# Kernel optimization log

Hardware: AMD Instinct MI355X
Metric: run time of the kernel (lower is better)

## Reference

```python
import jax, jax.numpy as jnp
import numpy as np

FULL_SCALE = 256
THRESH = 15.0  # full_scale > 128 -> distance_threshold = 15


def bilinear_sample(img, x, y):
    # img: [C,Hi,Wi]; x,y: [...] in [-1,1]; align_corners=False, zero padding
    C, Hi, Wi = img.shape
    xg = ((x + 1.0) * Wi - 1.0) / 2.0
    yg = ((y + 1.0) * Hi - 1.0) / 2.0
    x0 = jnp.floor(xg).astype(jnp.int32); x1 = x0 + 1
    y0 = jnp.floor(yg).astype(jnp.int32); y1 = y0 + 1
    wx = xg - x0.astype(img.dtype); wy = yg - y0.astype(img.dtype)

    def gather(yi, xi):
        valid = (yi >= 0) & (yi < Hi) & (xi >= 0) & (xi < Wi)
        yc = jnp.clip(yi, 0, Hi - 1); xc = jnp.clip(xi, 0, Wi - 1)
        return img[:, yc, xc] * valid[None].astype(img.dtype)

    return (gather(y0, x0) * ((1 - wy) * (1 - wx))[None]
            + gather(y0, x1) * ((1 - wy) * wx)[None]
            + gather(y1, x0) * (wy * (1 - wx))[None]
            + gather(y1, x1) * (wy * wx)[None])  # [C, ...]


def setup_inputs() -> dict:
    key = jax.random.key(0)
    k1, k2 = jax.random.split(key)
    image_x = jax.random.normal(k1, (1, 64, 256, 256), dtype=jnp.float32)
    all_edges = jax.random.uniform(k2, (8, 32, 4), dtype=jnp.float32)
    return {"image_x": image_x, "all_edges": all_edges}


def reference(image_x, all_edges):
    H = W = FULL_SCALE
    rows = jnp.arange(H, dtype=image_x.dtype)
    cols = jnp.arange(W, dtype=image_x.dtype)
    Vs, Us = jnp.meshgrid(rows, cols, indexing='ij')
    UV = jnp.stack([Vs, Us], axis=-1)  # [H,W,2] as (row, col), matches torch UVs

    def per_group(edges):
        e = edges * FULL_SCALE
        e0, e1 = e[:, :2], e[:, 2:4]
        d = e1 - e0                                    # [E,2]
        L = jnp.sqrt((d * d).sum(-1))                  # [E]
        dn = d / jnp.maximum(L, 1e-4)[:, None]
        nrm = jnp.stack([dn[:, 1], -dn[:, 0]], -1)     # normals
        diff = UV[:, :, None, :] - e0                  # [H,W,E,2]
        nd = jnp.abs((diff * nrm).sum(-1))             # normal distances [H,W,E]
        dd = (diff * dn).sum(-1) / jnp.maximum(L, 1e-4)  # direction distances
        near0 = jnp.sqrt((diff * diff).sum(-1)) <= THRESH
        near1 = jnp.sqrt(((UV[:, :, None, :] - e1) ** 2).sum(-1)) <= THRESH
        m = ((nd <= THRESH) & (dd <= 1) & (dd >= 0)) | near0 | near1  # all_edge_mask
        edge_mask = m.any(-1)                          # [H,W]
        off = jnp.minimum(dd, 1.0 - dd)                # point offsets
        mf = m.astype(image_x.dtype)
        pinfo = (off * mf).sum(-1) / jnp.maximum(mf.sum(-1), 1e-4)  # [H,W]
        return edge_mask, pinfo

    edge_mask, pinfo = jax.vmap(per_group)(all_edges)  # [G,H,W], [G,H,W]

    # grid_sample at every grid point (dense/masked equivalent of nonzero+gather);
    # torch swaps (v,u)->(u,v) so x = col, y = row, normalized p/size*2-1
    gx = (Us / FULL_SCALE) * 2.0 - 1.0
    gy = (Vs / FULL_SCALE) * 2.0 - 1.0
    sampled = bilinear_sample(image_x[0], gx, gy)      # [C,H,W]
    sampled = jnp.moveaxis(sampled, 0, -1)             # [H,W,C]

    G = all_edges.shape[0]
    feats = jnp.concatenate(
        [jnp.broadcast_to(sampled, (G,) + sampled.shape), pinfo[..., None]], axis=-1)
    feats = feats * edge_mask[..., None].astype(feats.dtype)  # zero non-edge pixels
    return feats, edge_mask
```

## Files before the change

kernel.cpp:

```cpp
#include <hip/hip_runtime.h>

#define HH 256
#define WW 256
#define CC 64
#define NG 8
#define NE 32
#define PX 32
#define THRESH 15.0f

typedef float f32x4 __attribute__((ext_vector_type(4)));

#define FEATS_ELEMS ((size_t)NG * HH * WW * 65)

#define IMG_ELEMS (CC * 2 * 33)

__global__ __launch_bounds__(256, 6) void fused_sparse_encoder(
    const float* __restrict__ img,
    const float* __restrict__ edges,
    float* __restrict__ out)
{
#pragma clang fp contract(off)
    __shared__ float  s_buf[66 * 65];
    __shared__ float4 s_k1[NG * NE];
    __shared__ float2 s_k2[NG * NE];
    __shared__ float  s_k3[NG * NE];
    __shared__ float  s_mask[NG * PX];
    __shared__ float  s_pinfo[NG * PX];

    const int tid = threadIdx.x;
    const int u0  = blockIdx.x * PX;
    const int v   = blockIdx.y;

    {
        const float4 e4 = reinterpret_cast<const float4*>(edges)[tid];
        const float e0v = e4.x * 256.0f;
        const float e0u = e4.y * 256.0f;
        const float e1v = e4.z * 256.0f;
        const float e1u = e4.w * 256.0f;
        const float d0 = e1v - e0v;
        const float d1 = e1u - e0u;
        const float L  = __fsqrt_rn(d0 * d0 + d1 * d1);
        const float Lm = fmaxf(L, 1e-4f);
        s_k1[tid] = make_float4(e0v, e0u, __fdiv_rn(d0, Lm), __fdiv_rn(d1, Lm));
        s_k2[tid] = make_float2(e1v, e1u);
        s_k3[tid] = Lm;
    }
    __syncthreads();

    float cbuf[17];
    #pragma unroll
    for (int t = 0; t < 17; ++t) {
        const int i = tid + t * 256;
        float val = 0.0f;
        if (i < IMG_ELEMS) {
            const int c  = i / 66;
            const int r  = i - c * 66;
            const int yy = r / 33;
            const int x  = r - yy * 33;
            const int gy = v - 1 + yy;
            const int gx = u0 - 1 + x;
            if (gy >= 0 && gx >= 0) {
                val = img[((size_t)c * HH + gy) * WW + gx];
            }
        }
        cbuf[t] = val;
    }

    {
        const int px = tid & (PX - 1);
        const int g  = tid >> 5;
        const float U = (float)(u0 + px);
        const float V = (float)v;
        float sm = 0.0f, cnt = 0.0f;
        bool any = false;
        for (int e = 0; e < NE; ++e) {
            const int idx = g * NE + e;
            const float4 k1 = s_k1[idx];
            const float2 k2 = s_k2[idx];
            const float  Lm = s_k3[idx];
            const float diff0 = V - k1.x;
            const float diff1 = U - k1.y;
            const float ndv = diff0 * k1.w - diff1 * k1.z;
            const float ddn = diff0 * k1.z + diff1 * k1.w;
            const float dd  = __fdiv_rn(ddn, Lm);
            const float r0sq = diff0 * diff0 + diff1 * diff1;
            const float f0 = V - k2.x;
            const float f1 = U - k2.y;
            const float r1sq = f0 * f0 + f1 * f1;
            const bool m = ((fabsf(ndv) <= THRESH) && (dd <= 1.0f) && (dd >= 0.0f))
                           || (r0sq <= 225.0f) || (r1sq <= 225.0f);
            if (m) {
                any = true;
                sm += fminf(dd, 1.0f - dd);
                cnt += 1.0f;
            }
        }
        const float pf = __fdiv_rn(sm, fmaxf(cnt, 1e-4f));
        const float mv = any ? 1.0f : 0.0f;
        s_mask[g * PX + px]  = mv;
        s_pinfo[g * PX + px] = pf;
        out[FEATS_ELEMS + ((size_t)g * HH + v) * WW + (u0 + px)] = mv;
    }

    #pragma unroll
    for (int t = 0; t < 17; ++t) {
        const int i = tid + t * 256;
        if (i < IMG_ELEMS) {
            const int c  = i / 66;
            const int r  = i - c * 66;
            const int yy = r / 33;
            const int x  = r - yy * 33;
            s_buf[(yy * 33 + x) * 65 + c] = cbuf[t];
        }
    }
    __syncthreads();

    const int wv   = tid >> 6;
    const int lane = tid & 63;
    float sreg[8];
    #pragma unroll
    for (int i = 0; i < 8; ++i) {
        const int p = wv * 8 + i;
        sreg[i] = s_buf[(p) * 65 + lane] * 0.25f
                + s_buf[(p + 1) * 65 + lane] * 0.25f
                + s_buf[(33 + p) * 65 + lane] * 0.25f
                + s_buf[(34 + p) * 65 + lane] * 0.25f;
    }
    __syncthreads();

    #pragma unroll
    for (int i = 0; i < 8; ++i) {
        const int p = wv * 8 + i;
        s_buf[p * 65 + lane] = sreg[i];
    }
    __syncthreads();

    for (int g = 0; g < NG; ++g) {
        const float* msk = &s_mask[g * PX];
        const float* pin = &s_pinfo[g * PX];
        float* gout = out + (((size_t)g * HH + v) * WW + u0) * 65;
        #pragma unroll
        for (int k = 0; k < 3; ++k) {
            const int q = tid + k * 256;
            if (q < 520) {
                const int f  = q * 4;
                const int p0 = (int)((unsigned)f / 65u);
                const int b  = (p0 + 1) * 65 - f;
                const float4 tv = *reinterpret_cast<const float4*>(&s_buf[f]);
                const float m0  = msk[p0];
                const float m1  = msk[(b < 4) ? (p0 + 1) : p0];
                const float pi0 = pin[p0];
                f32x4 r;
                r.x = ((b == 1) ? pi0 : tv.x) * ((0 < b) ? m0 : m1);
                r.y = ((b == 2) ? pi0 : tv.y) * ((1 < b) ? m0 : m1);
                r.z = ((b == 3) ? pi0 : tv.z) * ((2 < b) ? m0 : m1);
                r.w = ((b == 4) ? pi0 : tv.w) * ((3 < b) ? m0 : m1);
                __builtin_nontemporal_store(r, reinterpret_cast<f32x4*>(&gout[f]));
            }
        }
    }
}

extern "C" void kernel_launch(void* const* d_in, const int* in_sizes, int n_in,
                              void* d_out, int out_size, void* d_ws, size_t ws_size,
                              hipStream_t stream) {
    const float* img   = (const float*)d_in[0];
    const float* edges = (const float*)d_in[1];
    float* out = (float*)d_out;
    dim3 grid(WW / PX, HH);
    fused_sparse_encoder<<<grid, 256, 0, stream>>>(img, edges, out);
}
```

Before: 40.39 us.

## Make each wavefront own an 8-pixel strip to remove block barriers

Each 64-lane wavefront now handles its own 8-pixel strip. It loads its own 9-column halo of the image tile into a private shared-memory strip, computes edge masks for those 8 pixels across all 8 groups, and writes all group outputs for the strip. This removes the three block-wide __syncthreads between the transpose, averaging and store phases. The cost is redundant halo loads (9 columns per 8 pixels instead of 33 per 32), more shared memory per block, and launch bounds lowered from 6 to 5 blocks per CU. Output stores are now issued per wave, each covering contiguous 8-pixel runs per group.

```diff
diff --git a/kernel.cpp b/kernel.cpp
--- a/kernel.cpp
+++ b/kernel.cpp
@@ -12,24 +12,27 @@
 
 #define FEATS_ELEMS ((size_t)NG * HH * WW * 65)
 
-#define IMG_ELEMS (CC * 2 * 33)
+#define STRIP_PAD 1172
+#define STRIP_LOAD (CC * 2 * 9)
 
-__global__ __launch_bounds__(256, 6) void fused_sparse_encoder(
+__global__ __launch_bounds__(256, 5) void fused_sparse_encoder(
     const float* __restrict__ img,
     const float* __restrict__ edges,
     float* __restrict__ out)
 {
 #pragma clang fp contract(off)
-    __shared__ float  s_buf[66 * 65];
     __shared__ float4 s_k1[NG * NE];
     __shared__ float2 s_k2[NG * NE];
     __shared__ float  s_k3[NG * NE];
-    __shared__ float  s_mask[NG * PX];
-    __shared__ float  s_pinfo[NG * PX];
+    __shared__ float  s_strip[4][STRIP_PAD];
+    __shared__ float  s_m[4][64];
+    __shared__ float  s_p[4][64];
 
-    const int tid = threadIdx.x;
-    const int u0  = blockIdx.x * PX;
-    const int v   = blockIdx.y;
+    const int tid  = threadIdx.x;
+    const int w    = tid >> 6;
+    const int lane = tid & 63;
+    const int u0   = blockIdx.x * PX;
+    const int v    = blockIdx.y;
 
     {
         const float4 e4 = reinterpret_cast<const float4*>(edges)[tid];
@@ -47,29 +50,29 @@
     }
     __syncthreads();
 
-    float cbuf[17];
+    const int gx0 = u0 + 8 * w - 1;
+    float cbuf[18];
     #pragma unroll
-    for (int t = 0; t < 17; ++t) {
-        const int i = tid + t * 256;
+    for (int t = 0; t < 18; ++t) {
+        const int i  = lane + t * 64;
+        const unsigned ui = (unsigned)i;
+        const int c  = (int)(ui / 18u);
+        const int r  = i - c * 18;
+        const int yy = (r >= 9) ? 1 : 0;
+        const int x  = r - yy * 9;
+        const int gy = v - 1 + yy;
+        const int gx = gx0 + x;
         float val = 0.0f;
-        if (i < IMG_ELEMS) {
-            const int c  = i / 66;
-            const int r  = i - c * 66;
-            const int yy = r / 33;
-            const int x  = r - yy * 33;
-            const int gy = v - 1 + yy;
-            const int gx = u0 - 1 + x;
-            if (gy >= 0 && gx >= 0) {
-                val = img[((size_t)c * HH + gy) * WW + gx];
-            }
+        if (gy >= 0 && gx >= 0) {
+            val = img[((size_t)c * HH + gy) * WW + gx];
         }
         cbuf[t] = val;
     }
 
     {
-        const int px = tid & (PX - 1);
-        const int g  = tid >> 5;
-        const float U = (float)(u0 + px);
+        const int g   = lane >> 3;
+        const int pxl = lane & 7;
+        const float U = (float)(u0 + 8 * w + pxl);
         const float V = (float)v;
         float sm = 0.0f, cnt = 0.0f;
         bool any = false;
@@ -97,64 +100,58 @@
         }
         const float pf = __fdiv_rn(sm, fmaxf(cnt, 1e-4f));
         const float mv = any ? 1.0f : 0.0f;
-        s_mask[g * PX + px]  = mv;
-        s_pinfo[g * PX + px] = pf;
-        out[FEATS_ELEMS + ((size_t)g * HH + v) * WW + (u0 + px)] = mv;
+        s_m[w][lane] = mv;
+        s_p[w][lane] = pf;
+        out[FEATS_ELEMS + ((size_t)g * HH + v) * WW + (u0 + 8 * w + pxl)] = mv;
     }
 
     #pragma unroll
-    for (int t = 0; t < 17; ++t) {
-        const int i = tid + t * 256;
-        if (i < IMG_ELEMS) {
-            const int c  = i / 66;
-            const int r  = i - c * 66;
-            const int yy = r / 33;
-            const int x  = r - yy * 33;
-            s_buf[(yy * 33 + x) * 65 + c] = cbuf[t];
-        }
+    for (int t = 0; t < 18; ++t) {
+        const int i  = lane + t * 64;
+        const unsigned ui = (unsigned)i;
+        const int c  = (int)(ui / 18u);
+        const int r  = i - c * 18;
+        const int yy = (r >= 9) ? 1 : 0;
+        const int x  = r - yy * 9;
+        s_strip[w][(yy * 9 + x) * 65 + c] = cbuf[t];
     }
-    __syncthreads();
 
-    const int wv   = tid >> 6;
-    const int lane = tid & 63;
     float sreg[8];
     #pragma unroll
     for (int i = 0; i < 8; ++i) {
-        const int p = wv * 8 + i;
-        sreg[i] = s_buf[(p) * 65 + lane] * 0.25f
-                + s_buf[(p + 1) * 65 + lane] * 0.25f
-                + s_buf[(33 + p) * 65 + lane] * 0.25f
-                + s_buf[(34 + p) * 65 + lane] * 0.25f;
+        sreg[i] = s_strip[w][(i) * 65 + lane] * 0.25f
+                + s_strip[w][(i + 1) * 65 + lane] * 0.25f
+                + s_strip[w][(9 + i) * 65 + lane] * 0.25f
+                + s_strip[w][(10 + i) * 65 + lane] * 0.25f;
     }
-    __syncthreads();
 
     #pragma unroll
     for (int i = 0; i < 8; ++i) {
-        const int p = wv * 8 + i;
-        s_buf[p * 65 + lane] = sreg[i];
+        s_strip[w][i * 65 + lane] = sreg[i];
     }
-    __syncthreads();
 
-    for (int g = 0; g < NG; ++g) {
-        const float* msk = &s_mask[g * PX];
-        const float* pin = &s_pinfo[g * PX];
-        float* gout = out + (((size_t)g * HH + v) * WW + u0) * 65;
+    {
+        const size_t arow = ((size_t)v * WW + u0 + 8 * w);
         #pragma unroll
-        for (int k = 0; k < 3; ++k) {
-            const int q = tid + k * 256;
-            if (q < 520) {
+        for (int t = 0; t < 17; ++t) {
+            const int j = lane + t * 64;
+            if (j < 1040) {
+                const unsigned uj = (unsigned)j;
+                const int g  = (int)(uj / 130u);
+                const int q  = j - g * 130;
                 const int f  = q * 4;
                 const int p0 = (int)((unsigned)f / 65u);
                 const int b  = (p0 + 1) * 65 - f;
-                const float4 tv = *reinterpret_cast<const float4*>(&s_buf[f]);
-                const float m0  = msk[p0];
-                const float m1  = msk[(b < 4) ? (p0 + 1) : p0];
-                const float pi0 = pin[p0];
+                const f32x4 tv = *reinterpret_cast<const f32x4*>(&s_strip[w][f]);
+                const float m0  = s_m[w][g * 8 + p0];
+                const float m1  = s_m[w][g * 8 + ((b < 4) ? (p0 + 1) : p0)];
+                const float pi0 = s_p[w][g * 8 + p0];
                 f32x4 r;
                 r.x = ((b == 1) ? pi0 : tv.x) * ((0 < b) ? m0 : m1);
                 r.y = ((b == 2) ? pi0 : tv.y) * ((1 < b) ? m0 : m1);
                 r.z = ((b == 3) ? pi0 : tv.z) * ((2 < b) ? m0 : m1);
                 r.w = ((b == 4) ? pi0 : tv.w) * ((3 < b) ? m0 : m1);
+                float* gout = out + ((size_t)g * HH * WW + arow) * 65;
                 __builtin_nontemporal_store(r, reinterpret_cast<f32x4*>(&gout[f]));
             }
         }
```

After: 48.95 us. 21.2% more time.

## Process two pixel tiles per block with software-pipelined image loads

Applied to the files above, without the earlier changes.

Each block now handles two adjacent 32-pixel tiles. It issues the global image loads for the second tile before sampling and storing the first, and double-buffers the mask and pinfo arrays. The per-thread store index math is hoisted out of the group loop and reused. This amortizes the edge-parameter setup and hides global load latency behind compute and stores. The cost is half as many blocks, more register pressure (launch bounds lowered to 4 blocks) and more barriers per block.

```diff
diff --git a/kernel.cpp b/kernel.cpp
--- a/kernel.cpp
+++ b/kernel.cpp
@@ -14,7 +14,7 @@
 
 #define IMG_ELEMS (CC * 2 * 33)
 
-__global__ __launch_bounds__(256, 6) void fused_sparse_encoder(
+__global__ __launch_bounds__(256, 4) void fused_sparse_encoder(
     const float* __restrict__ img,
     const float* __restrict__ edges,
     float* __restrict__ out)
@@ -24,12 +24,14 @@
     __shared__ float4 s_k1[NG * NE];
     __shared__ float2 s_k2[NG * NE];
     __shared__ float  s_k3[NG * NE];
-    __shared__ float  s_mask[NG * PX];
-    __shared__ float  s_pinfo[NG * PX];
-
-    const int tid = threadIdx.x;
-    const int u0  = blockIdx.x * PX;
-    const int v   = blockIdx.y;
+    __shared__ float  s_mask[2][NG * PX];
+    __shared__ float  s_pinfo[2][NG * PX];
+
+    const int tid  = threadIdx.x;
+    const int wv   = tid >> 6;
+    const int lane = tid & 63;
+    const int v    = blockIdx.y;
+    const int u00  = blockIdx.x * (2 * PX);
 
     {
         const float4 e4 = reinterpret_cast<const float4*>(edges)[tid];
@@ -47,26 +49,55 @@
     }
     __syncthreads();
 
+    int  e_f[3], e_p0[3], e_b[3];
+    bool e_on[3];
+    #pragma unroll
+    for (int k = 0; k < 3; ++k) {
+        const int q = tid + k * 256;
+        e_on[k] = (q < 520);
+        const int f  = q * 4;
+        const int p0 = (int)((unsigned)f / 65u);
+        e_f[k] = f; e_p0[k] = p0; e_b[k] = (p0 + 1) * 65 - f;
+    }
+
     float cbuf[17];
-    #pragma unroll
-    for (int t = 0; t < 17; ++t) {
-        const int i = tid + t * 256;
-        float val = 0.0f;
-        if (i < IMG_ELEMS) {
-            const int c  = i / 66;
-            const int r  = i - c * 66;
-            const int yy = r / 33;
-            const int x  = r - yy * 33;
-            const int gy = v - 1 + yy;
-            const int gx = u0 - 1 + x;
-            if (gy >= 0 && gx >= 0) {
-                val = img[((size_t)c * HH + gy) * WW + gx];
-            }
-        }
-        cbuf[t] = val;
-    }
-
-    {
+    float sreg[8];
+
+    auto issue_loads = [&](int u0) {
+        #pragma unroll
+        for (int t = 0; t < 17; ++t) {
+            const int i = tid + t * 256;
+            float val = 0.0f;
+            if (i < IMG_ELEMS) {
+                const int c  = i / 66;
+                const int r  = i - c * 66;
+                const int yy = r / 33;
+                const int x  = r - yy * 33;
+                const int gy = v - 1 + yy;
+                const int gx = u0 - 1 + x;
+                if (gy >= 0 && gx >= 0) {
+                    val = img[((size_t)c * HH + gy) * WW + gx];
+                }
+            }
+            cbuf[t] = val;
+        }
+    };
+
+    auto commit = [&]() {
+        #pragma unroll
+        for (int t = 0; t < 17; ++t) {
+            const int i = tid + t * 256;
+            if (i < IMG_ELEMS) {
+                const int c  = i / 66;
+                const int r  = i - c * 66;
+                const int yy = r / 33;
+                const int x  = r - yy * 33;
+                s_buf[(yy * 33 + x) * 65 + c] = cbuf[t];
+            }
+        }
+    };
+
+    auto phaseB = [&](int u0, int pb) {
         const int px = tid & (PX - 1);
         const int g  = tid >> 5;
         const float U = (float)(u0 + px);
@@ -97,68 +128,72 @@
         }
         const float pf = __fdiv_rn(sm, fmaxf(cnt, 1e-4f));
         const float mv = any ? 1.0f : 0.0f;
-        s_mask[g * PX + px]  = mv;
-        s_pinfo[g * PX + px] = pf;
+        s_mask[pb][g * PX + px]  = mv;
+        s_pinfo[pb][g * PX + px] = pf;
         out[FEATS_ELEMS + ((size_t)g * HH + v) * WW + (u0 + px)] = mv;
-    }
-
-    #pragma unroll
-    for (int t = 0; t < 17; ++t) {
-        const int i = tid + t * 256;
-        if (i < IMG_ELEMS) {
-            const int c  = i / 66;
-            const int r  = i - c * 66;
-            const int yy = r / 33;
-            const int x  = r - yy * 33;
-            s_buf[(yy * 33 + x) * 65 + c] = cbuf[t];
-        }
-    }
-    __syncthreads();
-
-    const int wv   = tid >> 6;
-    const int lane = tid & 63;
-    float sreg[8];
-    #pragma unroll
-    for (int i = 0; i < 8; ++i) {
-        const int p = wv * 8 + i;
-        sreg[i] = s_buf[(p) * 65 + lane] * 0.25f
-                + s_buf[(p + 1) * 65 + lane] * 0.25f
-                + s_buf[(33 + p) * 65 + lane] * 0.25f
-                + s_buf[(34 + p) * 65 + lane] * 0.25f;
-    }
-    __syncthreads();
-
-    #pragma unroll
-    for (int i = 0; i < 8; ++i) {
-        const int p = wv * 8 + i;
-        s_buf[p * 65 + lane] = sreg[i];
-    }
-    __syncthreads();
-
-    for (int g = 0; g < NG; ++g) {
-        const float* msk = &s_mask[g * PX];
-        const float* pin = &s_pinfo[g * PX];
-        float* gout = out + (((size_t)g * HH + v) * WW + u0) * 65;
-        #pragma unroll
-        for (int k = 0; k < 3; ++k) {
-            const int q = tid + k * 256;
-            if (q < 520) {
-                const int f  = q * 4;
-                const int p0 = (int)((unsigned)f / 65u);
-                const int b  = (p0 + 1) * 65 - f;
-                const float4 tv = *reinterpret_cast<const float4*>(&s_buf[f]);
-                const float m0  = msk[p0];
-                const float m1  = msk[(b < 4) ? (p0 + 1) : p0];
-                const float pi0 = pin[p0];
-                f32x4 r;
-                r.x = ((b == 1) ? pi0 : tv.x) * ((0 < b) ? m0 : m1);
-                r.y = ((b == 2) ? pi0 : tv.y) * ((1 < b) ? m0 : m1);
-                r.z = ((b == 3) ? pi0 : tv.z) * ((2 < b) ? m0 : m1);
-                r.w = ((b == 4) ? pi0 : tv.w) * ((3 < b) ? m0 : m1);
-                __builtin_nontemporal_store(r, reinterpret_cast<f32x4*>(&gout[f]));
-            }
-        }
-    }
+    };
+
+    auto sample = [&]() {
+        #pragma unroll
+        for (int i = 0; i < 8; ++i) {
+            const int p = wv * 8 + i;
+            sreg[i] = s_buf[(p) * 65 + lane] * 0.25f
+                    + s_buf[(p + 1) * 65 + lane] * 0.25f
+                    + s_buf[(33 + p) * 65 + lane] * 0.25f
+                    + s_buf[(34 + p) * 65 + lane] * 0.25f;
+        }
+    };
+
+    auto transpose = [&]() {
+        #pragma unroll
+        for (int i = 0; i < 8; ++i) {
+            s_buf[(wv * 8 + i) * 65 + lane] = sreg[i];
+        }
+    };
+
+    auto storeE = [&](int u0, int pb) {
+        for (int g = 0; g < NG; ++g) {
+            float* gout = out + (((size_t)g * HH + v) * WW + u0) * 65;
+            #pragma unroll
+            for (int k = 0; k < 3; ++k) {
+                if (e_on[k]) {
+                    const int f  = e_f[k];
+                    const int p0 = e_p0[k];
+                    const int b  = e_b[k];
+                    const f32x4 tv = *reinterpret_cast<const f32x4*>(&s_buf[f]);
+                    const float m0  = s_mask[pb][g * PX + p0];
+                    const float m1  = s_mask[pb][g * PX + ((b < 4) ? (p0 + 1) : p0)];
+                    const float pi0 = s_pinfo[pb][g * PX + p0];
+                    f32x4 r;
+                    r.x = ((b == 1) ? pi0 : tv.x) * ((0 < b) ? m0 : m1);
+                    r.y = ((b == 2) ? pi0 : tv.y) * ((1 < b) ? m0 : m1);
+                    r.z = ((b == 3) ? pi0 : tv.z) * ((2 < b) ? m0 : m1);
+                    r.w = ((b == 4) ? pi0 : tv.w) * ((3 < b) ? m0 : m1);
+                    __builtin_nontemporal_store(r, reinterpret_cast<f32x4*>(&gout[f]));
+                }
+            }
+        }
+    };
+
+    issue_loads(u00);
+    phaseB(u00, 0);
+    commit();
+    issue_loads(u00 + PX);
+    __syncthreads();
+    sample();
+    __syncthreads();
+    transpose();
+    __syncthreads();
+    storeE(u00, 0);
+    phaseB(u00 + PX, 1);
+    __syncthreads();
+    commit();
+    __syncthreads();
+    sample();
+    __syncthreads();
+    transpose();
+    __syncthreads();
+    storeE(u00 + PX, 1);
 }
 
 extern "C" void kernel_launch(void* const* d_in, const int* in_sizes, int n_in,
@@ -167,6 +202,6 @@
     const float* img   = (const float*)d_in[0];
     const float* edges = (const float*)d_in[1];
     float* out = (float*)d_out;
-    dim3 grid(WW / PX, HH);
+    dim3 grid(WW / (2 * PX), HH);
     fused_sparse_encoder<<<grid, 256, 0, stream>>>(img, edges, out);
 }
```

Measured after the change: 45.68 us. +13.1%, slower.

## Halve pixel tile width and hoist per-thread output tile loads out of group loop

Applied to the files above, without the earlier changes.

Shrinks the per-block pixel strip from 32 to 16, doubling the number of blocks, and sizes the image staging buffers to the smaller halo. The pooled sample tile now goes into a separate shared buffer, which removes one barrier. Each thread's float4 slice of the tile and its index math are computed once and reused across all 8 groups. The cost is that the edge-mask loop runs on only half the threads, and the halo rows are reloaded more often relative to useful work.

```diff
diff --git a/kernel.cpp b/kernel.cpp
--- a/kernel.cpp
+++ b/kernel.cpp
@@ -5,14 +5,15 @@
 #define CC 64
 #define NG 8
 #define NE 32
-#define PX 32
+#define PX 16
 #define THRESH 15.0f
 
 typedef float f32x4 __attribute__((ext_vector_type(4)));
 
 #define FEATS_ELEMS ((size_t)NG * HH * WW * 65)
 
-#define IMG_ELEMS (CC * 2 * 33)
+#define IMG_ROWS 34
+#define IMG_ELEMS (IMG_ROWS * CC)
 
 __global__ __launch_bounds__(256, 6) void fused_sparse_encoder(
     const float* __restrict__ img,
@@ -20,16 +21,19 @@
     float* __restrict__ out)
 {
 #pragma clang fp contract(off)
-    __shared__ float  s_buf[66 * 65];
+    __shared__ __align__(16) float s_buf[IMG_ROWS * 65];
+    __shared__ __align__(16) float s_t[PX * 65];
     __shared__ float4 s_k1[NG * NE];
     __shared__ float2 s_k2[NG * NE];
     __shared__ float  s_k3[NG * NE];
-    __shared__ float  s_mask[NG * PX];
-    __shared__ float  s_pinfo[NG * PX];
+    __shared__ float  s_m[NG * PX];
+    __shared__ float  s_p[NG * PX];
 
-    const int tid = threadIdx.x;
-    const int u0  = blockIdx.x * PX;
-    const int v   = blockIdx.y;
+    const int tid  = threadIdx.x;
+    const int wv   = tid >> 6;
+    const int lane = tid & 63;
+    const int u0   = blockIdx.x * PX;
+    const int v    = blockIdx.y;
 
     {
         const float4 e4 = reinterpret_cast<const float4*>(edges)[tid];
@@ -47,16 +51,16 @@
     }
     __syncthreads();
 
-    float cbuf[17];
+    float cbuf[9];
     #pragma unroll
-    for (int t = 0; t < 17; ++t) {
+    for (int t = 0; t < 9; ++t) {
         const int i = tid + t * 256;
         float val = 0.0f;
         if (i < IMG_ELEMS) {
-            const int c  = i / 66;
-            const int r  = i - c * 66;
-            const int yy = r / 33;
-            const int x  = r - yy * 33;
+            const int c  = i / IMG_ROWS;
+            const int r  = i - c * IMG_ROWS;
+            const int yy = (r >= 17) ? 1 : 0;
+            const int x  = r - yy * 17;
             const int gy = v - 1 + yy;
             const int gx = u0 - 1 + x;
             if (gy >= 0 && gx >= 0) {
@@ -66,9 +70,9 @@
         cbuf[t] = val;
     }
 
-    {
+    if (tid < 128) {
         const int px = tid & (PX - 1);
-        const int g  = tid >> 5;
+        const int g  = tid >> 4;
         const float U = (float)(u0 + px);
         const float V = (float)v;
         float sm = 0.0f, cnt = 0.0f;
@@ -97,66 +101,80 @@
         }
         const float pf = __fdiv_rn(sm, fmaxf(cnt, 1e-4f));
         const float mv = any ? 1.0f : 0.0f;
-        s_mask[g * PX + px]  = mv;
-        s_pinfo[g * PX + px] = pf;
+        s_m[g * PX + px] = mv;
+        s_p[g * PX + px] = pf;
         out[FEATS_ELEMS + ((size_t)g * HH + v) * WW + (u0 + px)] = mv;
     }
 
     #pragma unroll
-    for (int t = 0; t < 17; ++t) {
+    for (int t = 0; t < 9; ++t) {
         const int i = tid + t * 256;
         if (i < IMG_ELEMS) {
-            const int c  = i / 66;
-            const int r  = i - c * 66;
-            const int yy = r / 33;
-            const int x  = r - yy * 33;
-            s_buf[(yy * 33 + x) * 65 + c] = cbuf[t];
+            const int c  = i / IMG_ROWS;
+            const int r  = i - c * IMG_ROWS;
+            const int yy = (r >= 17) ? 1 : 0;
+            const int x  = r - yy * 17;
+            s_buf[(yy * 17 + x) * 65 + c] = cbuf[t];
         }
     }
     __syncthreads();
 
-    const int wv   = tid >> 6;
-    const int lane = tid & 63;
-    float sreg[8];
+    float sreg[4];
     #pragma unroll
-    for (int i = 0; i < 8; ++i) {
-        const int p = wv * 8 + i;
+    for (int i = 0; i < 4; ++i) {
+        const int p = wv * 4 + i;
         sreg[i] = s_buf[(p) * 65 + lane] * 0.25f
                 + s_buf[(p + 1) * 65 + lane] * 0.25f
-                + s_buf[(33 + p) * 65 + lane] * 0.25f
-                + s_buf[(34 + p) * 65 + lane] * 0.25f;
+                + s_buf[(17 + p) * 65 + lane] * 0.25f
+                + s_buf[(18 + p) * 65 + lane] * 0.25f;
+    }
+
+    #pragma unroll
+    for (int i = 0; i < 4; ++i) {
+        s_t[(wv * 4 + i) * 65 + lane] = sreg[i];
     }
     __syncthreads();
 
-    #pragma unroll
-    for (int i = 0; i < 8; ++i) {
-        const int p = wv * 8 + i;
-        s_buf[p * 65 + lane] = sreg[i];
-    }
-    __syncthreads();
+    const int f0  = tid * 4;
+    const int p00 = (int)((unsigned)f0 / 65u);
+    const int b0  = (p00 + 1) * 65 - f0;
+    const int pA0 = p00;
+    const int pB0 = (b0 < 4) ? (p00 + 1) : p00;
+
+    const bool on1 = (tid < 4);
+    const int f1  = (tid + 256) * 4;
+    const int p01 = (int)((unsigned)f1 / 65u);
+    const int b1  = (p01 + 1) * 65 - f1;
+    const int pA1 = p01;
+    const int pB1 = (b1 < 4) ? (p01 + 1) : p01;
+
+    const f32x4 tv0 = *reinterpret_cast<const f32x4*>(&s_t[f0]);
+    f32x4 tv1;
+    if (on1) tv1 = *reinterpret_cast<const f32x4*>(&s_t[f1]);
 
     for (int g = 0; g < NG; ++g) {
-        const float* msk = &s_mask[g * PX];
-        const float* pin = &s_pinfo[g * PX];
         float* gout = out + (((size_t)g * HH + v) * WW + u0) * 65;
-        #pragma unroll
-        for (int k = 0; k < 3; ++k) {
-            const int q = tid + k * 256;
-            if (q < 520) {
-                const int f  = q * 4;
-                const int p0 = (int)((unsigned)f / 65u);
-                const int b  = (p0 + 1) * 65 - f;
-                const float4 tv = *reinterpret_cast<const float4*>(&s_buf[f]);
-                const float m0  = msk[p0];
-                const float m1  = msk[(b < 4) ? (p0 + 1) : p0];
-                const float pi0 = pin[p0];
-                f32x4 r;
-                r.x = ((b == 1) ? pi0 : tv.x) * ((0 < b) ? m0 : m1);
-                r.y = ((b == 2) ? pi0 : tv.y) * ((1 < b) ? m0 : m1);
-                r.z = ((b == 3) ? pi0 : tv.z) * ((2 < b) ? m0 : m1);
-                r.w = ((b == 4) ? pi0 : tv.w) * ((3 < b) ? m0 : m1);
-                __builtin_nontemporal_store(r, reinterpret_cast<f32x4*>(&gout[f]));
-            }
+        {
+            const float m0 = s_m[g * PX + pA0];
+            const float m1 = s_m[g * PX + pB0];
+            const float pi = s_p[g * PX + pA0];
+            f32x4 r;
+            r.x = ((b0 == 1) ? pi : tv0.x) * ((0 < b0) ? m0 : m1);
+            r.y = ((b0 == 2) ? pi : tv0.y) * ((1 < b0) ? m0 : m1);
+            r.z = ((b0 == 3) ? pi : tv0.z) * ((2 < b0) ? m0 : m1);
+            r.w = ((b0 == 4) ? pi : tv0.w) * ((3 < b0) ? m0 : m1);
+            __builtin_nontemporal_store(r, reinterpret_cast<f32x4*>(&gout[f0]));
+        }
+        if (on1) {
+            const float m0 = s_m[g * PX + pA1];
+            const float m1 = s_m[g * PX + pB1];
+            const float pi = s_p[g * PX + pA1];
+            f32x4 r;
+            r.x = ((b1 == 1) ? pi : tv1.x) * ((0 < b1) ? m0 : m1);
+            r.y = ((b1 == 2) ? pi : tv1.y) * ((1 < b1) ? m0 : m1);
+            r.z = ((b1 == 3) ? pi : tv1.z) * ((2 < b1) ? m0 : m1);
+            r.w = ((b1 == 4) ? pi : tv1.w) * ((3 < b1) ? m0 : m1);
+            __builtin_nontemporal_store(r, reinterpret_cast<f32x4*>(&gout[f1]));
         }
     }
 }
```

Measured after the change: 43.01 us. 6.5% more time.
